# Performance work log

Hardware: AMD Instinct MI355X
Metric: run time of the kernel (lower is better)

Reference implementation:

```python
import jax, jax.numpy as jnp
import numpy as np

B, S, E, H = 4, 2048, 1024, 16
HD = E // H  # head_dim = 64


def setup_inputs() -> dict:
    key = jax.random.key(0)
    k1, k2, k3, k4 = jax.random.split(key, 4)
    x = jax.random.normal(k1, (B, S, E), dtype=jnp.float32)
    Wqkv = jax.random.normal(k2, (3 * E, E), dtype=jnp.float32) * (E ** -0.5)
    Wo = jax.random.normal(k3, (E, E), dtype=jnp.float32) * (E ** -0.5)
    bo = jax.random.normal(k4, (E,), dtype=jnp.float32) * 0.01
    return {"x": x, "Wqkv": Wqkv, "Wo": Wo, "bo": bo}


def reference(x, Wqkv, Wo, bo):
    b, s, e = x.shape
    # qkv projection (nn.Linear without bias: x @ W^T) -> (b, s, 3e)
    qkv = x @ Wqkv.T
    # reshape (b, s, H, 3*HD) -> (b, H, s, 3*HD), then chunk into q,k,v
    qkv = qkv.reshape(b, s, H, 3 * HD).transpose(0, 2, 1, 3)
    q, k, v = jnp.split(qkv, 3, axis=-1)  # each (b, H, s, HD)
    scale = 1.0 / jnp.sqrt(jnp.asarray(HD, dtype=x.dtype))
    scores = jnp.einsum('bhqd,bhkd->bhqk', q, k) * scale  # (b, H, s, s)
    causal = jnp.tril(jnp.ones((s, s), dtype=bool))
    scores = jnp.where(causal, scores, -jnp.inf)
    probs = jax.nn.softmax(scores, axis=-1)
    out = jnp.einsum('bhqk,bhkd->bhqd', probs, v)  # (b, H, s, HD)
    out = out.transpose(0, 2, 1, 3).reshape(b, s, e)
    return out @ Wo.T + bo
```

## Files before the change

kernel.cpp:

```cpp
#include <hip/hip_runtime.h>
#include <stdint.h>

#define Bn 4
#define Sn 2048
#define En 1024
#define Hn 16
#define HDn 64

typedef __bf16 bf16;
typedef __bf16 bf16x4 __attribute__((ext_vector_type(4)));
typedef __bf16 bf16x8 __attribute__((ext_vector_type(8)));
typedef float  f32x4  __attribute__((ext_vector_type(4)));
typedef float  f32x16 __attribute__((ext_vector_type(16)));
typedef uint32_t u32x4 __attribute__((ext_vector_type(4)));
typedef int      i32x2 __attribute__((ext_vector_type(2)));

#define GLDS(gp, lp) __builtin_amdgcn_global_load_lds( \
    (const __attribute__((address_space(1))) void*)(gp), \
    (__attribute__((address_space(3))) void*)(lp), 16, 0, 0)

#define BAR() __builtin_amdgcn_s_barrier()
#define WLG() do { asm volatile("s_waitcnt lgkmcnt(0)" ::: "memory"); \
                   __builtin_amdgcn_sched_barrier(0); } while (0)
#define WVM4() asm volatile("s_waitcnt vmcnt(4)" ::: "memory")

static __device__ __forceinline__ i32x2 plsw(uint32_t a, uint32_t b)
{
    return __builtin_amdgcn_permlane32_swap((int)a, (int)b, false, false);
}

__global__ __launch_bounds__(256) void cvt_all(
    const float* __restrict__ x, const float* __restrict__ wqkv,
    const float* __restrict__ wo,
    bf16* __restrict__ xb, bf16* __restrict__ wqkvb, bf16* __restrict__ wob)
{
    const int n1 = Bn*Sn*En/4;
    const int n2 = 3*En*En/4;
    const int n3 = En*En/4;
    const int tot = n1 + n2 + n3;
    for (int i = blockIdx.x*256 + threadIdx.x; i < tot; i += gridDim.x*256) {
        const float* src; bf16* dst; int j;
        if (i < n1)           { src = x;    dst = xb;    j = i; }
        else if (i < n1 + n2) { src = wqkv; dst = wqkvb; j = i - n1; }
        else                  { src = wo;   dst = wob;   j = i - n1 - n2; }
        float4 f = reinterpret_cast<const float4*>(src)[j];
        bf16x4 o;
        o[0] = (bf16)f.x; o[1] = (bf16)f.y; o[2] = (bf16)f.z; o[3] = (bf16)f.w;
        reinterpret_cast<bf16x4*>(dst)[j] = o;
    }
}

template<int MODE>
__global__ __launch_bounds__(512, 2) void gemm256(
    const bf16* __restrict__ Ag, const bf16* __restrict__ Bw,
    int M, int N, int K,
    bf16* __restrict__ q_out, bf16* __restrict__ k_out, bf16* __restrict__ v_out,
    float* __restrict__ c_out, const float* __restrict__ bias)
{
    __shared__ __align__(16) bf16 lA[2 * 256 * 64];
    __shared__ __align__(16) bf16 lB[2 * 256 * 64];

    const int tid  = threadIdx.x;
    const int lane = tid & 63;
    const int w    = tid >> 6;
    const int wm = w >> 2, wn = w & 3;
    const int lr = lane & 15, lg = lane >> 4;
    const int m0 = blockIdx.y * 256;
    const int n0 = blockIdx.x * 256;
    const int NT = K >> 6;
    const int niter = NT >> 1;

    const int srow = tid >> 3;
    const int sck  = (tid & 7) ^ ((tid >> 3) & 7);

    f32x4 acc[8][4] = {};

    auto stageA = [&](int t, int half) {
        const int ts = t < NT ? t : NT - 1;
        bf16* Ld = lA + ((t & 1) ? 16384 : 0) + (half*128 + w*8) * 64;
        const bf16* S = Ag + (size_t)(m0 + half*128 + srow) * K + ts*64 + sck*8;
        GLDS(S, Ld);
        GLDS(S + (size_t)64 * K, Ld + 64 * 64);
    };
    auto stageB = [&](int t, int half) {
        const int ts = t < NT ? t : NT - 1;
        bf16* Ld = lB + ((t & 1) ? 16384 : 0) + (half*128 + w*8) * 64;
        const bf16* S = Bw + (size_t)(n0 + half*128 + srow) * K + ts*64 + sck*8;
        GLDS(S, Ld);
        GLDS(S + (size_t)64 * K, Ld + 64 * 64);
    };
    auto ldA4 = [&](bf16x8 (&a)[4][2], const bf16* Lb, int qm) {
        #pragma unroll
        for (int ii = 0; ii < 4; ++ii) {
            const bf16* p = Lb + (wm*128 + qm*64 + ii*16 + lr) * 64;
            #pragma unroll
            for (int kk = 0; kk < 2; ++kk)
                a[ii][kk] = *reinterpret_cast<const bf16x8*>(p + (((kk << 2) + lg) ^ (lr & 7)) * 8);
        }
    };
    auto ldB2 = [&](bf16x8 (&b)[2][2], const bf16* Lb, int qn) {
        #pragma unroll
        for (int j = 0; j < 2; ++j) {
            const bf16* p = Lb + (wn*64 + qn*32 + j*16 + lr) * 64;
            #pragma unroll
            for (int kk = 0; kk < 2; ++kk)
                b[j][kk] = *reinterpret_cast<const bf16x8*>(p + (((kk << 2) + lg) ^ (lr & 7)) * 8);
        }
    };
    auto mmac = [&](const bf16x8 (&a)[4][2], const bf16x8 (&b)[2][2], int qm, int qn) {
        __builtin_amdgcn_s_setprio(1);
        #pragma unroll
        for (int ii = 0; ii < 4; ++ii)
            #pragma unroll
            for (int j = 0; j < 2; ++j)
                #pragma unroll
                for (int kk = 0; kk < 2; ++kk)
                    acc[qm*4 + ii][qn*2 + j] = __builtin_amdgcn_mfma_f32_16x16x32_bf16(
                        a[ii][kk], b[j][kk], acc[qm*4 + ii][qn*2 + j], 0, 0, 0);
        __builtin_amdgcn_s_setprio(0);
    };

    stageA(0, 0); stageA(0, 1); stageB(0, 0); stageB(0, 1);
    stageB(1, 0); stageB(1, 1);
    WVM4(); BAR();

    const bf16* A0 = lA;          const bf16* A1 = lA + 16384;
    const bf16* B0l = lB;         const bf16* B1l = lB + 16384;
    bf16x8 a[4][2], b0[2][2], b1[2][2];

    for (int i = 0; i < niter; ++i) {
        const int t = 2 * i;
        ldA4(a, A0, 0); ldB2(b0, B0l, 0);
        stageA(t + 1, 0);
        BAR(); WLG();
        mmac(a, b0, 0, 0);
        BAR();
        ldB2(b1, B0l, 1);
        stageA(t + 1, 1);
        BAR(); WLG();
        mmac(a, b1, 0, 1);
        BAR();
        ldA4(a, A0, 1);
        stageB(t + 2, 0);
        BAR(); WLG();
        mmac(a, b0, 1, 0);
        BAR();
        stageB(t + 2, 1);
        WVM4(); BAR();
        mmac(a, b1, 1, 1);
        BAR();
        ldA4(a, A1, 0); ldB2(b0, B1l, 0);
        stageA(t + 2, 0);
        BAR(); WLG();
        mmac(a, b0, 0, 0);
        BAR();
        ldB2(b1, B1l, 1);
        stageA(t + 2, 1);
        BAR(); WLG();
        mmac(a, b1, 0, 1);
        BAR();
        ldA4(a, A1, 1);
        stageB(t + 3, 0);
        BAR(); WLG();
        mmac(a, b0, 1, 0);
        BAR();
        stageB(t + 3, 1);
        WVM4(); BAR();
        mmac(a, b1, 1, 1);
        BAR();
    }

    #pragma unroll
    for (int ii = 0; ii < 8; ++ii) {
        #pragma unroll
        for (int j = 0; j < 4; ++j) {
            const int colb = n0 + wn*64 + j*16 + lr;
            #pragma unroll
            for (int r = 0; r < 4; ++r) {
                const int rowb = m0 + wm*128 + ii*16 + lg*4 + r;
                const float v = acc[ii][j][r];
                if (MODE == 0) {
                    const int bb = rowb >> 11, s = rowb & (Sn - 1);
                    const int h = colb / 192, rr = colb - h*192;
                    const int wq = rr >> 6, hd = rr & 63;
                    const size_t off = (((size_t)(bb*Hn + h))*Sn + s)*HDn + hd;
                    const bf16 bv = (bf16)v;
                    if (wq == 0)      q_out[off] = bv;
                    else if (wq == 1) k_out[off] = bv;
                    else              v_out[off] = bv;
                } else {
                    c_out[(size_t)rowb*N + colb] = v + bias[colb];
                }
            }
        }
    }
}

__global__ __launch_bounds__(256) void gemm_bt(
    const bf16* __restrict__ A, const bf16* __restrict__ Bw,
    int M, int N, int K,
    float* __restrict__ c_out, const float* __restrict__ bias)
{
    __shared__ bf16 lA[128*64];
    __shared__ bf16 lB[128*64];
    const int tid  = threadIdx.x;
    const int lane = tid & 63;
    const int wv   = tid >> 6;
    const int wm = wv >> 1, wn = wv & 1;
    const int m0 = blockIdx.y * 128;
    const int n0 = blockIdx.x * 128;
    const int lr = lane & 15, lg = lane >> 4;

    f32x4 acc[4][4] = {};

    const int rowA = wv*8 + (lane>>3);
    const int col8 = (lane&7)*8;

    for (int k0 = 0; k0 < K; k0 += 64) {
        #pragma unroll
        for (int c = 0; c < 4; ++c) {
            int row = c*32 + rowA;
            GLDS(A  + (size_t)(m0+row)*K + k0 + col8, lA + (c*32 + wv*8)*64);
            GLDS(Bw + (size_t)(n0+row)*K + k0 + col8, lB + (c*32 + wv*8)*64);
        }
        __syncthreads();
        #pragma unroll
        for (int kk = 0; kk < 64; kk += 32) {
            bf16x8 af[4], bfv[4];
            #pragma unroll
            for (int i = 0; i < 4; ++i)
                af[i] = *reinterpret_cast<const bf16x8*>(lA + (wm*64 + i*16 + lr)*64 + kk + lg*8);
            #pragma unroll
            for (int j = 0; j < 4; ++j)
                bfv[j] = *reinterpret_cast<const bf16x8*>(lB + (wn*64 + j*16 + lr)*64 + kk + lg*8);
            #pragma unroll
            for (int i = 0; i < 4; ++i)
                #pragma unroll
                for (int j = 0; j < 4; ++j)
                    acc[i][j] = __builtin_amdgcn_mfma_f32_16x16x32_bf16(af[i], bfv[j], acc[i][j], 0, 0, 0);
        }
        __syncthreads();
    }

    #pragma unroll
    for (int i = 0; i < 4; ++i) {
        #pragma unroll
        for (int j = 0; j < 4; ++j) {
            const int colb = n0 + wn*64 + j*16 + lr;
            #pragma unroll
            for (int r = 0; r < 4; ++r) {
                const int rowb = m0 + wm*64 + i*16 + lg*4 + r;
                c_out[(size_t)rowb*N + colb] = acc[i][j][r] + bias[colb];
            }
        }
    }
}

static __device__ __forceinline__ uint32_t pkbf(float lo, float hi)
{
    uint16_t a = __builtin_bit_cast(uint16_t, (bf16)lo);
    uint16_t b = __builtin_bit_cast(uint16_t, (bf16)hi);
    return (uint32_t)a | ((uint32_t)b << 16);
}

__global__ __launch_bounds__(512) void attn_fwd(
    const bf16* __restrict__ Q, const bf16* __restrict__ Kg, const bf16* __restrict__ Vg,
    bf16* __restrict__ O)
{
    __shared__ __align__(16) bf16 Kl[2][64*64];
    __shared__ __align__(16) bf16 Vt[2][64*64];

    const int tid  = threadIdx.x;
    const int lane = tid & 63;
    const int w    = tid >> 6;
    const int col  = lane & 31;
    const int hv   = lane >> 5;
    const int bh   = blockIdx.x;
    const int qb   = (gridDim.y - 1) - blockIdx.y;
    const int q0w  = qb*256 + w*32;
    const int qg   = q0w + col;

    const bf16* Qb = Q  + (size_t)bh*Sn*HDn;
    const bf16* Kb = Kg + (size_t)bh*Sn*HDn;
    const bf16* Vb = Vg + (size_t)bh*Sn*HDn;

    bf16x8 aq[4];
    #pragma unroll
    for (int ks = 0; ks < 4; ++ks)
        aq[ks] = *reinterpret_cast<const bf16x8*>(Qb + (size_t)qg*HDn + ks*16 + hv*8);

    f32x16 ov[2] = {};
    const float S2 = 0.18033688011112042f;
    float l_run = 0.f;

    const int skey = tid >> 3;
    const int scc  = tid & 7;
    const int ksw  = scc ^ (skey & 7);

    const int nst = 2*(qb+1);
    for (int sti = 0; sti < nst; ++sti) {
        const int k0 = sti*128;
        __syncthreads();
        GLDS(Kb + (size_t)(k0 + skey)*HDn + ksw*8,      &Kl[0][0] + (size_t)w*512);
        GLDS(Kb + (size_t)(k0 + 64 + skey)*HDn + ksw*8, &Kl[1][0] + (size_t)w*512);
        {
            bf16x8 v0 = *reinterpret_cast<const bf16x8*>(Vb + (size_t)(k0 + skey)*HDn + scc*8);
            bf16x8 v1 = *reinterpret_cast<const bf16x8*>(Vb + (size_t)(k0 + 64 + skey)*HDn + scc*8);
            #pragma unroll
            for (int j = 0; j < 8; ++j) {
                const int chunk = (scc*8 + j)*8 + ((skey>>3) ^ scc);
                Vt[0][chunk*8 + (skey&7)] = v0[j];
                Vt[1][chunk*8 + (skey&7)] = v1[j];
            }
        }
        __syncthreads();

        #pragma unroll
        for (int sub = 0; sub < 2; ++sub) {
            const int k0s = k0 + sub*64;
            if (k0s > q0w + 31) continue;

            f32x16 st[2] = {};
            #pragma unroll
            for (int kb = 0; kb < 2; ++kb) {
                const int key = kb*32 + col;
                #pragma unroll
                for (int ks = 0; ks < 4; ++ks) {
                    const int chunk = key*8 + ((ks*2 + hv) ^ (key & 7));
                    bf16x8 kf = *reinterpret_cast<const bf16x8*>(&Kl[sub][0] + chunk*8);
                    st[kb] = __builtin_amdgcn_mfma_f32_32x32x16_bf16(kf, aq[ks], st[kb], 0, 0, 0);
                }
            }

            if (k0s + 63 > q0w) {
                #pragma unroll
                for (int kb = 0; kb < 2; ++kb)
                    #pragma unroll
                    for (int r = 0; r < 16; ++r) {
                        const int keyg = k0s + kb*32 + (r&3) + 8*(r>>2) + 4*hv;
                        if (keyg > qg) st[kb][r] = -1e30f;
                    }
            }

            uint32_t wpk[2][8];
            float lsum = 0.f;
            #pragma unroll
            for (int kb = 0; kb < 2; ++kb) {
                float pr[8];
                #pragma unroll
                for (int i = 0; i < 8; ++i) {
                    const float e0 = exp2f(fmaf(st[kb][2*i],   S2, -8.0f));
                    const float e1 = exp2f(fmaf(st[kb][2*i+1], S2, -8.0f));
                    pr[i] = e0 + e1;
                    wpk[kb][i] = pkbf(e0, e1);
                }
                pr[0] += pr[4]; pr[1] += pr[5]; pr[2] += pr[6]; pr[3] += pr[7];
                pr[0] += pr[2]; pr[1] += pr[3];
                lsum += pr[0] + pr[1];
            }
            l_run += lsum;

            bf16x8 pB[4];
            #pragma unroll
            for (int s = 0; s < 4; ++s) {
                const int kb = s >> 1, ls = s & 1;
                i32x2 r02 = plsw(wpk[kb][4*ls+0], wpk[kb][4*ls+2]);
                i32x2 r13 = plsw(wpk[kb][4*ls+1], wpk[kb][4*ls+3]);
                u32x4 pwv = { (uint32_t)r02[0], (uint32_t)r13[0],
                              (uint32_t)r02[1], (uint32_t)r13[1] };
                pB[s] = __builtin_bit_cast(bf16x8, pwv);
            }

            #pragma unroll
            for (int s = 0; s < 4; ++s) {
                #pragma unroll
                for (int hb = 0; hb < 2; ++hb) {
                    const int hd = hb*32 + col;
                    const int chunk = hd*8 + ((s*2 + hv) ^ ((hd>>3) & 7));
                    bf16x8 vf = *reinterpret_cast<const bf16x8*>(&Vt[sub][0] + chunk*8);
                    ov[hb] = __builtin_amdgcn_mfma_f32_32x32x16_bf16(vf, pB[s], ov[hb], 0, 0, 0);
                }
            }
        }
    }

    const float lt  = l_run + __shfl_xor(l_run, 32);
    const float inv = 1.0f / lt;
    const int b = bh >> 4, hh = bh & 15;
    bf16* Ob = O + ((size_t)(b*Sn + qg))*En + hh*HDn;
    #pragma unroll
    for (int hb = 0; hb < 2; ++hb)
        #pragma unroll
        for (int g = 0; g < 4; ++g) {
            bf16x4 o4;
            #pragma unroll
            for (int r4 = 0; r4 < 4; ++r4)
                o4[r4] = (bf16)(ov[hb][g*4 + r4] * inv);
            *reinterpret_cast<bf16x4*>(Ob + hb*32 + g*8 + 4*hv) = o4;
        }
}

extern "C" void kernel_launch(void* const* d_in, const int* in_sizes, int n_in,
                              void* d_out, int out_size, void* d_ws, size_t ws_size,
                              hipStream_t stream)
{
    (void)in_sizes; (void)n_in; (void)out_size; (void)ws_size;
    const float* x    = (const float*)d_in[0];
    const float* Wqkv = (const float*)d_in[1];
    const float* Wo   = (const float*)d_in[2];
    const float* bo   = (const float*)d_in[3];
    float* out = (float*)d_out;

    const size_t nBS = (size_t)Bn*Sn;
    char* ws = (char*)d_ws;
    bf16* xb    = (bf16*)ws; ws += nBS*En*2;
    bf16* wqkvb = (bf16*)ws; ws += (size_t)3*En*En*2;
    bf16* wob   = (bf16*)ws; ws += (size_t)En*En*2;
    bf16* Qb    = (bf16*)ws; ws += nBS*En*2;
    bf16* Kb    = (bf16*)ws; ws += nBS*En*2;
    bf16* Vb    = (bf16*)ws; ws += nBS*En*2;
    bf16* AO    = (bf16*)ws; ws += nBS*En*2;

    cvt_all<<<2048, 256, 0, stream>>>(x, Wqkv, Wo, xb, wqkvb, wob);

    gemm256<0><<<dim3(3*En/256, nBS/256), 512, 0, stream>>>(
        xb, wqkvb, (int)nBS, 3*En, En, Qb, Kb, Vb, nullptr, nullptr);

    attn_fwd<<<dim3(Bn*Hn, Sn/256), 512, 0, stream>>>(Qb, Kb, Vb, AO);

    gemm_bt<<<dim3(En/128, nBS/128), 256, 0, stream>>>(
        AO, wob, (int)nBS, En, En, out, bo);
}
```

Before: 182.9 us.

## Replace output-projection GEMM with double-buffered swizzled 128x256 pipelined kernel

```diff
diff --git a/kernel.cpp b/kernel.cpp
--- a/kernel.cpp
+++ b/kernel.cpp
@@ -196,61 +196,131 @@
     }
 }
 
-__global__ __launch_bounds__(256) void gemm_bt(
-    const bf16* __restrict__ A, const bf16* __restrict__ Bw,
+__global__ __launch_bounds__(512, 1) void gemm128(
+    const bf16* __restrict__ Ag, const bf16* __restrict__ Bw,
     int M, int N, int K,
     float* __restrict__ c_out, const float* __restrict__ bias)
 {
-    __shared__ bf16 lA[128*64];
-    __shared__ bf16 lB[128*64];
+    __shared__ __align__(16) bf16 lA[2 * 128 * 64];
+    __shared__ __align__(16) bf16 lB[2 * 256 * 64];
+
     const int tid  = threadIdx.x;
     const int lane = tid & 63;
-    const int wv   = tid >> 6;
-    const int wm = wv >> 1, wn = wv & 1;
+    const int w    = tid >> 6;
+    const int wm = w >> 2, wn = w & 3;
+    const int lr = lane & 15, lg = lane >> 4;
     const int m0 = blockIdx.y * 128;
-    const int n0 = blockIdx.x * 128;
-    const int lr = lane & 15, lg = lane >> 4;
+    const int n0 = blockIdx.x * 256;
+    const int NT = K >> 6;
+    const int niter = NT >> 1;
+
+    const int srow = tid >> 3;
+    const int sck  = (tid & 7) ^ ((tid >> 3) & 7);
 
     f32x4 acc[4][4] = {};
 
-    const int rowA = wv*8 + (lane>>3);
-    const int col8 = (lane&7)*8;
-
-    for (int k0 = 0; k0 < K; k0 += 64) {
-        #pragma unroll
-        for (int c = 0; c < 4; ++c) {
-            int row = c*32 + rowA;
-            GLDS(A  + (size_t)(m0+row)*K + k0 + col8, lA + (c*32 + wv*8)*64);
-            GLDS(Bw + (size_t)(n0+row)*K + k0 + col8, lB + (c*32 + wv*8)*64);
-        }
-        __syncthreads();
-        #pragma unroll
-        for (int kk = 0; kk < 64; kk += 32) {
-            bf16x8 af[4], bfv[4];
-            #pragma unroll
-            for (int i = 0; i < 4; ++i)
-                af[i] = *reinterpret_cast<const bf16x8*>(lA + (wm*64 + i*16 + lr)*64 + kk + lg*8);
-            #pragma unroll
-            for (int j = 0; j < 4; ++j)
-                bfv[j] = *reinterpret_cast<const bf16x8*>(lB + (wn*64 + j*16 + lr)*64 + kk + lg*8);
-            #pragma unroll
-            for (int i = 0; i < 4; ++i)
+    auto stageA = [&](int t) {
+        const int ts = t < NT ? t : NT - 1;
+        bf16* Ld = lA + ((t & 1) ? 8192 : 0) + (w*8) * 64;
+        const bf16* S = Ag + (size_t)(m0 + srow) * K + ts*64 + sck*8;
+        GLDS(S, Ld);
+        GLDS(S + (size_t)64 * K, Ld + 64 * 64);
+    };
+    auto stageB = [&](int t, int half) {
+        const int ts = t < NT ? t : NT - 1;
+        bf16* Ld = lB + ((t & 1) ? 16384 : 0) + (half*128 + w*8) * 64;
+        const bf16* S = Bw + (size_t)(n0 + half*128 + srow) * K + ts*64 + sck*8;
+        GLDS(S, Ld);
+        GLDS(S + (size_t)64 * K, Ld + 64 * 64);
+    };
+    auto ldA2 = [&](bf16x8 (&a)[2][2], const bf16* Lb, int qm) {
+        #pragma unroll
+        for (int ii = 0; ii < 2; ++ii) {
+            const bf16* p = Lb + (wm*64 + qm*32 + ii*16 + lr) * 64;
+            #pragma unroll
+            for (int kk = 0; kk < 2; ++kk)
+                a[ii][kk] = *reinterpret_cast<const bf16x8*>(p + (((kk << 2) + lg) ^ (lr & 7)) * 8);
+        }
+    };
+    auto ldB2 = [&](bf16x8 (&b)[2][2], const bf16* Lb, int qn) {
+        #pragma unroll
+        for (int j = 0; j < 2; ++j) {
+            const bf16* p = Lb + (wn*64 + qn*32 + j*16 + lr) * 64;
+            #pragma unroll
+            for (int kk = 0; kk < 2; ++kk)
+                b[j][kk] = *reinterpret_cast<const bf16x8*>(p + (((kk << 2) + lg) ^ (lr & 7)) * 8);
+        }
+    };
+    auto mmac = [&](const bf16x8 (&a)[2][2], const bf16x8 (&b)[2][2], int qm, int qn) {
+        __builtin_amdgcn_s_setprio(1);
+        #pragma unroll
+        for (int ii = 0; ii < 2; ++ii)
+            #pragma unroll
+            for (int j = 0; j < 2; ++j)
                 #pragma unroll
-                for (int j = 0; j < 4; ++j)
-                    acc[i][j] = __builtin_amdgcn_mfma_f32_16x16x32_bf16(af[i], bfv[j], acc[i][j], 0, 0, 0);
-        }
-        __syncthreads();
+                for (int kk = 0; kk < 2; ++kk)
+                    acc[qm*2 + ii][qn*2 + j] = __builtin_amdgcn_mfma_f32_16x16x32_bf16(
+                        a[ii][kk], b[j][kk], acc[qm*2 + ii][qn*2 + j], 0, 0, 0);
+        __builtin_amdgcn_s_setprio(0);
+    };
+
+    stageA(0); stageB(0, 0); stageB(0, 1);
+    stageB(1, 0); stageB(1, 1);
+    WVM4(); BAR();
+
+    const bf16* A0 = lA;          const bf16* A1 = lA + 8192;
+    const bf16* B0l = lB;         const bf16* B1l = lB + 16384;
+    bf16x8 a[2][2], b0[2][2], b1[2][2];
+
+    for (int i = 0; i < niter; ++i) {
+        const int t = 2 * i;
+        ldA2(a, A0, 0); ldB2(b0, B0l, 0);
+        stageA(t + 1);
+        BAR(); WLG();
+        mmac(a, b0, 0, 0);
+        BAR();
+        ldB2(b1, B0l, 1);
+        BAR(); WLG();
+        mmac(a, b1, 0, 1);
+        BAR();
+        ldA2(a, A0, 1);
+        stageB(t + 2, 0);
+        BAR(); WLG();
+        mmac(a, b0, 1, 0);
+        BAR();
+        stageB(t + 2, 1);
+        WVM4(); BAR();
+        mmac(a, b1, 1, 1);
+        BAR();
+        ldA2(a, A1, 0); ldB2(b0, B1l, 0);
+        stageA(t + 2);
+        BAR(); WLG();
+        mmac(a, b0, 0, 0);
+        BAR();
+        ldB2(b1, B1l, 1);
+        BAR(); WLG();
+        mmac(a, b1, 0, 1);
+        BAR();
+        ldA2(a, A1, 1);
+        stageB(t + 3, 0);
+        BAR(); WLG();
+        mmac(a, b0, 1, 0);
+        BAR();
+        stageB(t + 3, 1);
+        WVM4(); BAR();
+        mmac(a, b1, 1, 1);
+        BAR();
     }
 
     #pragma unroll
-    for (int i = 0; i < 4; ++i) {
+    for (int ii = 0; ii < 4; ++ii) {
         #pragma unroll
         for (int j = 0; j < 4; ++j) {
             const int colb = n0 + wn*64 + j*16 + lr;
             #pragma unroll
             for (int r = 0; r < 4; ++r) {
-                const int rowb = m0 + wm*64 + i*16 + lg*4 + r;
-                c_out[(size_t)rowb*N + colb] = acc[i][j][r] + bias[colb];
+                const int rowb = m0 + wm*64 + ii*16 + lg*4 + r;
+                c_out[(size_t)rowb*N + colb] = acc[ii][j][r] + bias[colb];
             }
         }
     }
@@ -428,6 +498,6 @@
 
     attn_fwd<<<dim3(Bn*Hn, Sn/256), 512, 0, stream>>>(Qb, Kb, Vb, AO);
 
-    gemm_bt<<<dim3(En/128, nBS/128), 256, 0, stream>>>(
+    gemm128<<<dim3(En/256, nBS/128), 512, 0, stream>>>(
         AO, wob, (int)nBS, En, En, out, bo);
 }
```

Measured after the change: 184.1 us. About the same (+0.6%).
